# Optimization experiments

Measured on AMD Instinct MI355X. Metric: run time of the kernel, lower is better.

Reference implementation:

```python
import jax, jax.numpy as jnp
import numpy as np

N_NODES = 100000
N_EDGES = 800000
DIMS = [(768, 64), (64, 32), (32, 16), (16, 5)]


def setup_inputs() -> dict:
    key = jax.random.key(0)
    ks = jax.random.split(key, 3 + 3 * len(DIMS))
    inp = {
        "x": jax.random.normal(ks[0], (N_NODES, DIMS[0][0]), jnp.float32),
        "edge_index": jax.random.randint(ks[1], (2, N_EDGES), 0, N_NODES),
        "edge_weight": jax.random.uniform(ks[2], (N_EDGES,), jnp.float32),
    }
    for i, (di, do) in enumerate(DIMS, start=1):
        s = 1.0 / np.sqrt(di)
        k0, k1, k2 = ks[3 * i], ks[3 * i + 1], ks[3 * i + 2]
        inp[f"W{i}l"] = jax.random.uniform(k0, (di, do), jnp.float32, -s, s)
        inp[f"W{i}r"] = jax.random.uniform(k1, (di, do), jnp.float32, -s, s)
        inp[f"b{i}"] = jax.random.uniform(k2, (do,), jnp.float32, -s, s)
    return inp


def _sage_conv(h, src, dst, inv_deg, Wl, Wr, b):
    # SAGEConv (mean aggregation): lin_l(mean_{j->i} h_j) + lin_r(h_i)
    agg = jax.ops.segment_sum(h[src], dst, num_segments=h.shape[0]) * inv_deg[:, None]
    return agg @ Wl + h @ Wr + b


def reference(x, edge_index, edge_weight,
              W1l, W1r, b1, W2l, W2r, b2, W3l, W3r, b3, W4l, W4r, b4):
    # edge_weight is accepted (matches original forward) but PyG SAGEConv mean
    # aggregation ignores it. Dropout is identity (deterministic eval reference).
    src, dst = edge_index[0], edge_index[1]
    deg = jax.ops.segment_sum(jnp.ones((src.shape[0],), x.dtype), dst,
                              num_segments=x.shape[0])
    inv_deg = jnp.where(deg > 0, 1.0 / deg, 0.0)
    h = jax.nn.relu(_sage_conv(x, src, dst, inv_deg, W1l, W1r, b1))
    h = jax.nn.relu(_sage_conv(h, src, dst, inv_deg, W2l, W2r, b2))
    h = jax.nn.relu(_sage_conv(h, src, dst, inv_deg, W3l, W3r, b3))
    return _sage_conv(h, src, dst, inv_deg, W4l, W4r, b4)
```

## Files before the change

kernel.cpp:

```cpp
#include <hip/hip_runtime.h>

using half8 = __attribute__((ext_vector_type(8))) _Float16;
using f32x4 = __attribute__((ext_vector_type(4))) float;

typedef __attribute__((address_space(3))) unsigned int lds_uint;
typedef __attribute__((address_space(1))) const unsigned int glb_uint;
__device__ __forceinline__ void async_copy16(const void* g, void* l) {
  __builtin_amdgcn_global_load_lds((glb_uint*)g, (lds_uint*)l, 16, 0, 0);
}

__device__ __forceinline__ void raw_barrier() {
  asm volatile("" ::: "memory");
  __builtin_amdgcn_s_barrier();
  asm volatile("" ::: "memory");
}

__global__ void zero_kernel(int4* __restrict__ p, int n4) {
  int i = blockIdx.x * 256 + threadIdx.x;
  if (i < n4) p[i] = make_int4(0, 0, 0, 0);
}

__global__ void prep_all_kernel(const float* __restrict__ W1l, const float* __restrict__ W1r,
                                const float* __restrict__ W2l, const float* __restrict__ W2r,
                                const float* __restrict__ W3l, const float* __restrict__ W3r,
                                const float* __restrict__ W4l, const float* __restrict__ W4r,
                                _Float16* __restrict__ w1, _Float16* __restrict__ w2,
                                _Float16* __restrict__ w3, _Float16* __restrict__ w4) {
  int i = blockIdx.x * 256 + threadIdx.x;
  if (i < 98304) {
    int c = i / 768, k = i - c * 768;
    float v = (c < 64) ? W1l[k * 64 + c] : W1r[k * 64 + (c - 64)];
    w1[i] = (_Float16)v;
  } else if (i < 98304 + 4096) {
    int j = i - 98304;
    int c = j >> 6, k = j & 63;
    float v = (c < 32) ? W2l[k * 32 + c] : W2r[k * 32 + (c - 32)];
    w2[j] = (_Float16)v;
  } else if (i < 98304 + 4096 + 1024) {
    int j = i - (98304 + 4096);
    int c = j >> 5, k = j & 31;
    float v = (c < 16) ? W3l[k * 16 + c] : W3r[k * 16 + (c - 16)];
    w3[j] = (_Float16)v;
  } else if (i < 98304 + 4096 + 1024 + 512) {
    int j = i - (98304 + 4096 + 1024);
    int c = j >> 5, k = j & 31;
    float v = 0.f;
    if (k < 16) {
      if (c < 5) v = W4l[k * 5 + c];
      else if (c < 10) v = W4r[k * 5 + (c - 5)];
    }
    w4[j] = (_Float16)v;
  }
}

__global__ void deg_kernel(const int* __restrict__ dst, int* __restrict__ cnt, int e) {
  int i = blockIdx.x * 256 + threadIdx.x;
  if (i < e) atomicAdd(&cnt[dst[i]], 1);
}

__global__ void scan1_kernel(const int* __restrict__ cnt, int* __restrict__ off,
                             int* __restrict__ bsum, float* __restrict__ invd, int nodes) {
  __shared__ int sh[256];
  int tid = threadIdx.x;
  int base = blockIdx.x * 1024 + tid * 4;
  int a0 = (base + 0 < nodes) ? cnt[base + 0] : 0;
  int a1 = (base + 1 < nodes) ? cnt[base + 1] : 0;
  int a2 = (base + 2 < nodes) ? cnt[base + 2] : 0;
  int a3 = (base + 3 < nodes) ? cnt[base + 3] : 0;
  if (base + 0 < nodes) invd[base + 0] = a0 > 0 ? 1.0f / (float)a0 : 0.f;
  if (base + 1 < nodes) invd[base + 1] = a1 > 0 ? 1.0f / (float)a1 : 0.f;
  if (base + 2 < nodes) invd[base + 2] = a2 > 0 ? 1.0f / (float)a2 : 0.f;
  if (base + 3 < nodes) invd[base + 3] = a3 > 0 ? 1.0f / (float)a3 : 0.f;
  int s3 = a0 + a1 + a2 + a3;
  sh[tid] = s3;
  __syncthreads();
  for (int d = 1; d < 256; d <<= 1) {
    int v = (tid >= d) ? sh[tid - d] : 0;
    __syncthreads();
    sh[tid] += v;
    __syncthreads();
  }
  int excl = sh[tid] - s3;
  if (base + 0 <= nodes) off[base + 0] = excl;
  if (base + 1 <= nodes) off[base + 1] = excl + a0;
  if (base + 2 <= nodes) off[base + 2] = excl + a0 + a1;
  if (base + 3 <= nodes) off[base + 3] = excl + a0 + a1 + a2;
  if (tid == 255) bsum[blockIdx.x] = sh[255];
}

__global__ void scan2_kernel(int* __restrict__ bsum, int nb) {
  __shared__ int sh[128];
  int tid = threadIdx.x;
  int v = (tid < nb) ? bsum[tid] : 0;
  sh[tid] = v;
  __syncthreads();
  for (int d = 1; d < 128; d <<= 1) {
    int u = (tid >= d) ? sh[tid - d] : 0;
    __syncthreads();
    sh[tid] += u;
    __syncthreads();
  }
  if (tid < nb) bsum[tid] = sh[tid] - v;
}

__global__ void scan3_kernel(int* __restrict__ off, const int* __restrict__ bsum, int ntot) {
  int i = blockIdx.x * 256 + threadIdx.x;
  if (i < ntot) off[i] += bsum[i >> 10];
}

__global__ void sortfill_kernel(const int* __restrict__ src, const int* __restrict__ dst,
                                const int* __restrict__ off, int* __restrict__ cur,
                                int* __restrict__ csr, int e) {
  int i = blockIdx.x * 256 + threadIdx.x;
  if (i < e) {
    int d = dst[i];
    int pos = atomicAdd(&cur[d], 1);
    csr[off[d] + pos] = src[i];
  }
}

__global__ __launch_bounds__(256, 3) void gemm1_kernel(
    const float* __restrict__ x,
    const _Float16* __restrict__ w16,
    const float* __restrict__ bias,
    _Float16* __restrict__ p, _Float16* __restrict__ q, int n) {
  constexpr int DI = 768, BK = 32, NT = DI / BK;
  __shared__ float aS[3][64 * BK];
  __shared__ _Float16 bS[3][128 * BK];
  int t = threadIdx.x;
  int lane = t & 63, w = t >> 6;
  int lm = lane & 15, lk = lane >> 4;
  int m0 = blockIdx.x * 64;

  const float* agp[2];
  int abase[2];
#pragma unroll
  for (int j = 0; j < 2; ++j) {
    int g = j * 256 + w * 64 + lane;
    int row = g >> 3, gi = g & 7;
    int gj = gi ^ (row & 7);
    int grow = m0 + row;
    if (grow >= n) grow = n - 1;
    agp[j] = x + (size_t)grow * DI + gj * 4;
    abase[j] = (j * 256 + w * 64) * 4;
  }
  const _Float16* bgp[2];
  int bbase[2];
#pragma unroll
  for (int j = 0; j < 2; ++j) {
    int g = j * 256 + w * 64 + lane;
    int c = g >> 2, gi = g & 3;
    int gj = gi ^ ((c >> 1) & 3);
    bgp[j] = w16 + (size_t)c * DI + gj * 8;
    bbase[j] = (j * 256 + w * 64) * 8;
  }

  f32x4 acc[8];
#pragma unroll
  for (int ni = 0; ni < 8; ++ni) acc[ni] = (f32x4){0.f, 0.f, 0.f, 0.f};

  int r0l = w * 16 + lm;
  int sw = r0l & 7;
  int bsw = (lk ^ ((lm >> 1) & 3)) << 3;

  auto stage = [&](int buf, int kc) {
#pragma unroll
    for (int j = 0; j < 2; ++j) async_copy16(agp[j] + kc, &aS[buf][abase[j]]);
#pragma unroll
    for (int j = 0; j < 2; ++j) async_copy16(bgp[j] + kc, &bS[buf][bbase[j]]);
  };

  auto compute_tile = [&](const float* ab, const _Float16* bb) {
    f32x4 v0a = *(const f32x4*)(ab + r0l * 32 + (((lk * 2 + 0) ^ sw) << 2));
    f32x4 v0b = *(const f32x4*)(ab + r0l * 32 + (((lk * 2 + 1) ^ sw) << 2));
    half8 a0;
#pragma unroll
    for (int j = 0; j < 4; ++j) {
      a0[j] = (_Float16)v0a[j];
      a0[4 + j] = (_Float16)v0b[j];
    }
#pragma unroll
    for (int ni = 0; ni < 8; ++ni) {
      half8 b = *(const half8*)(bb + (ni * 16 + lm) * 32 + bsw);
      acc[ni] = __builtin_amdgcn_mfma_f32_16x16x32_f16(a0, b, acc[ni], 0, 0, 0);
    }
  };

  stage(0, 0);
  stage(1, BK);

  for (int ts = 0; ts < NT; ++ts) {
    if (ts + 2 < NT) {
      stage((ts + 2) % 3, (ts + 2) * BK);
      asm volatile("s_waitcnt vmcnt(8)" ::: "memory");
    } else if (ts + 1 < NT) {
      asm volatile("s_waitcnt vmcnt(4)" ::: "memory");
    } else {
      asm volatile("s_waitcnt vmcnt(0)" ::: "memory");
    }
    raw_barrier();
    int cur = ts % 3;
    compute_tile(aS[cur], bS[cur]);
    raw_barrier();
  }

#pragma unroll
  for (int ni = 0; ni < 8; ++ni) {
    int col = ni * 16 + lm;
#pragma unroll
    for (int j = 0; j < 4; ++j) {
      int row = m0 + w * 16 + lk * 4 + j;
      if (row < n) {
        float v = acc[ni][j];
        if (col < 64) p[(size_t)row * 64 + col] = (_Float16)v;
        else q[(size_t)row * 64 + (col - 64)] = (_Float16)(v + bias[col - 64]);
      }
    }
  }
}

template <int DIR, int DIP, int PSI, int NC, int NCR, int DO, int PSO>
__global__ __launch_bounds__(256) void fused_agg_gemm_kernel(
    const _Float16* __restrict__ pin, const _Float16* __restrict__ qin,
    const int* __restrict__ off, const int* __restrict__ csr, const float* __restrict__ invd,
    const _Float16* __restrict__ w16, const float* __restrict__ bias,
    _Float16* __restrict__ pout, _Float16* __restrict__ qout, int n) {
  constexpr int SP = DIP + 8;
  constexpr int C8 = DIR / 8;
  constexpr int CT = C8 / 2;
  constexpr int NF = NC / 16;
  __shared__ _Float16 hs[128 * SP];
  int t = threadIdx.x;
  int node_l = t >> 1, half = t & 1;
  int node = blockIdx.x * 128 + node_l;

  if (node < n) {
    int e0 = off[node], e1 = off[node + 1];
    const half8* p8 = (const half8*)pin;
    float s[CT][8];
#pragma unroll
    for (int c = 0; c < CT; ++c)
#pragma unroll
      for (int j = 0; j < 8; ++j) s[c][j] = 0.f;
    int e = e0;
    for (; e + 2 <= e1; e += 2) {
      int i0 = csr[e], i1 = csr[e + 1];
      half8 v0[CT], v1[CT];
#pragma unroll
      for (int c = 0; c < CT; ++c) v0[c] = p8[(size_t)i0 * PSI + half * CT + c];
#pragma unroll
      for (int c = 0; c < CT; ++c) v1[c] = p8[(size_t)i1 * PSI + half * CT + c];
#pragma unroll
      for (int c = 0; c < CT; ++c)
#pragma unroll
        for (int j = 0; j < 8; ++j) {
          s[c][j] += (float)v0[c][j];
          s[c][j] += (float)v1[c][j];
        }
    }
    if (e < e1) {
      int i0 = csr[e];
#pragma unroll
      for (int c = 0; c < CT; ++c) {
        half8 v = p8[(size_t)i0 * PSI + half * CT + c];
#pragma unroll
        for (int j = 0; j < 8; ++j) s[c][j] += (float)v[j];
      }
    }
    float id = invd[node];
#pragma unroll
    for (int c = 0; c < CT; ++c) {
      half8 qv = ((const half8*)qin)[(size_t)node * PSI + half * CT + c];
      half8 o;
#pragma unroll
      for (int j = 0; j < 8; ++j) o[j] = (_Float16)fmaxf(s[c][j] * id + (float)qv[j], 0.f);
      *(half8*)(hs + node_l * SP + (half * CT + c) * 8) = o;
    }
    if (DIP > DIR) {
      half8 z = {};
      *(half8*)(hs + node_l * SP + (C8 + half) * 8) = z;
    }
  }
  __syncthreads();

  int lane = t & 63, w = t >> 6;
  int lm = lane & 15, lk = lane >> 4;
  int r0l = w * 32 + lm, r1l = r0l + 16;
  const _Float16* wp = w16 + (size_t)lm * DIP + lk * 8;
  f32x4 acc[2][NF];
#pragma unroll
  for (int mi = 0; mi < 2; ++mi)
#pragma unroll
    for (int ni = 0; ni < NF; ++ni) acc[mi][ni] = (f32x4){0.f, 0.f, 0.f, 0.f};
#pragma unroll
  for (int kc = 0; kc < DIP; kc += 32) {
    half8 a0 = *(const half8*)(hs + r0l * SP + kc + lk * 8);
    half8 a1 = *(const half8*)(hs + r1l * SP + kc + lk * 8);
#pragma unroll
    for (int ni = 0; ni < NF; ++ni) {
      half8 b = *(const half8*)(wp + (size_t)ni * 16 * DIP + kc);
      acc[0][ni] = __builtin_amdgcn_mfma_f32_16x16x32_f16(a0, b, acc[0][ni], 0, 0, 0);
      acc[1][ni] = __builtin_amdgcn_mfma_f32_16x16x32_f16(a1, b, acc[1][ni], 0, 0, 0);
    }
  }
#pragma unroll
  for (int mi = 0; mi < 2; ++mi)
#pragma unroll
    for (int ni = 0; ni < NF; ++ni) {
      int col = ni * 16 + lm;
      if (col >= NCR) continue;
#pragma unroll
      for (int j = 0; j < 4; ++j) {
        int row = blockIdx.x * 128 + w * 32 + mi * 16 + lk * 4 + j;
        if (row < n) {
          float v = acc[mi][ni][j];
          if (col < DO) pout[(size_t)row * PSO + col] = (_Float16)v;
          else qout[(size_t)row * PSO + (col - DO)] = (_Float16)(v + bias[col - DO]);
        }
      }
    }
}

__global__ __launch_bounds__(256) void aggregate_last_kernel(
    const _Float16* __restrict__ p, const _Float16* __restrict__ q,
    const int* __restrict__ off, const int* __restrict__ csr,
    const float* __restrict__ invd, float* __restrict__ out, int n) {
  int node = blockIdx.x * 256 + threadIdx.x;
  if (node >= n) return;
  int e0 = off[node], e1 = off[node + 1];
  const half8* p8 = (const half8*)p;
  float s[8];
#pragma unroll
  for (int j = 0; j < 8; ++j) s[j] = 0.f;
  int e = e0;
  for (; e + 2 <= e1; e += 2) {
    half8 v0 = p8[csr[e]];
    half8 v1 = p8[csr[e + 1]];
#pragma unroll
    for (int j = 0; j < 8; ++j) {
      s[j] += (float)v0[j];
      s[j] += (float)v1[j];
    }
  }
  if (e < e1) {
    half8 v = p8[csr[e]];
#pragma unroll
    for (int j = 0; j < 8; ++j) s[j] += (float)v[j];
  }
  float id = invd[node];
  half8 qv = ((const half8*)q)[node];
#pragma unroll
  for (int j = 0; j < 5; ++j) out[(size_t)node * 5 + j] = s[j] * id + (float)qv[j];
}

extern "C" void kernel_launch(void* const* d_in, const int* in_sizes, int n_in,
                              void* d_out, int out_size, void* d_ws, size_t ws_size,
                              hipStream_t stream) {
  const float* x = (const float*)d_in[0];
  const int* ei = (const int*)d_in[1];
  const int E = in_sizes[1] / 2;
  const int* esrc = ei;
  const int* edst = ei + E;
  const float* W1l = (const float*)d_in[3];
  const float* W1r = (const float*)d_in[4];
  const float* b1 = (const float*)d_in[5];
  const float* W2l = (const float*)d_in[6];
  const float* W2r = (const float*)d_in[7];
  const float* b2 = (const float*)d_in[8];
  const float* W3l = (const float*)d_in[9];
  const float* W3r = (const float*)d_in[10];
  const float* b3 = (const float*)d_in[11];
  const float* W4l = (const float*)d_in[12];
  const float* W4r = (const float*)d_in[13];
  const float* b4 = (const float*)d_in[14];
  const int N = in_sizes[0] / 768;
  float* out = (float*)d_out;
  (void)n_in; (void)out_size; (void)ws_size;

  char* base = (char*)d_ws;
  size_t o = 0;
  auto alloc = [&](size_t bytes) -> void* {
    void* ptr = base + o;
    o = (o + bytes + 255) & ~(size_t)255;
    return ptr;
  };
  int* cnt = (int*)alloc((size_t)2 * N * 4);
  int* cur = cnt + N;
  int* off = (int*)alloc((size_t)(N + 1) * 4);
  int* bsum = (int*)alloc(1024);
  int* csr = (int*)alloc((size_t)E * 4);
  float* invd = (float*)alloc((size_t)N * 4);
  _Float16* w1 = (_Float16*)alloc((size_t)128 * 768 * 2);
  _Float16* w2 = (_Float16*)alloc((size_t)64 * 64 * 2);
  _Float16* w3 = (_Float16*)alloc((size_t)32 * 32 * 2);
  _Float16* w4 = (_Float16*)alloc((size_t)16 * 32 * 2);
  _Float16* P1 = (_Float16*)alloc((size_t)N * 64 * 2);
  _Float16* Q1 = (_Float16*)alloc((size_t)N * 64 * 2);
  _Float16* P2 = (_Float16*)alloc((size_t)N * 32 * 2);
  _Float16* Q2 = (_Float16*)alloc((size_t)N * 32 * 2);
  _Float16* P3 = (_Float16*)alloc((size_t)N * 16 * 2);
  _Float16* Q3 = (_Float16*)alloc((size_t)N * 16 * 2);
  _Float16* P4 = (_Float16*)alloc((size_t)N * 8 * 2);
  _Float16* Q4 = (_Float16*)alloc((size_t)N * 8 * 2);

  const int n4 = (2 * N + 3) / 4;
  zero_kernel<<<(n4 + 255) / 256, 256, 0, stream>>>((int4*)cnt, n4);
  prep_all_kernel<<<(98304 + 4096 + 1024 + 512 + 255) / 256, 256, 0, stream>>>(
      W1l, W1r, W2l, W2r, W3l, W3r, W4l, W4r, w1, w2, w3, w4);

  deg_kernel<<<(E + 255) / 256, 256, 0, stream>>>(edst, cnt, E);
  const int nb = (N + 1 + 1023) / 1024;
  scan1_kernel<<<nb, 256, 0, stream>>>(cnt, off, bsum, invd, N);
  scan2_kernel<<<1, 128, 0, stream>>>(bsum, nb);
  scan3_kernel<<<(N + 1 + 255) / 256, 256, 0, stream>>>(off, bsum, N + 1);
  sortfill_kernel<<<(E + 255) / 256, 256, 0, stream>>>(esrc, edst, off, cur, csr, E);

  gemm1_kernel<<<(N + 63) / 64, 256, 0, stream>>>(x, w1, b1, P1, Q1, N);
  const int gb = (N + 127) / 128;
  fused_agg_gemm_kernel<64, 64, 8, 64, 64, 32, 32>
      <<<gb, 256, 0, stream>>>(P1, Q1, off, csr, invd, w2, b2, P2, Q2, N);
  fused_agg_gemm_kernel<32, 32, 4, 32, 32, 16, 16>
      <<<gb, 256, 0, stream>>>(P2, Q2, off, csr, invd, w3, b3, P3, Q3, N);
  fused_agg_gemm_kernel<16, 32, 2, 16, 10, 5, 8>
      <<<gb, 256, 0, stream>>>(P3, Q3, off, csr, invd, w4, b4, P4, Q4, N);
  aggregate_last_kernel<<<(N + 255) / 256, 256, 0, stream>>>(P4, Q4, off, csr, invd, out, N);
}
```

Baseline: 273.5 us.

## Replace LDS-staged pipelined GEMM1 with direct global-to-register loads

Rewrites the first-layer GEMM to drop the triple-buffered async global-to-LDS staging and barriers, loading x rows and fp16 weights directly into registers per wave. Occupancy hint raised from 3 to 4 blocks per CU. This removes LDS traffic and barrier synchronisation but loses explicit prefetching and weight sharing across waves, relying on caches and occupancy to hide latency.

```diff
diff --git a/kernel.cpp b/kernel.cpp
--- a/kernel.cpp
+++ b/kernel.cpp
@@ -2,18 +2,6 @@
 
 using half8 = __attribute__((ext_vector_type(8))) _Float16;
 using f32x4 = __attribute__((ext_vector_type(4))) float;
-
-typedef __attribute__((address_space(3))) unsigned int lds_uint;
-typedef __attribute__((address_space(1))) const unsigned int glb_uint;
-__device__ __forceinline__ void async_copy16(const void* g, void* l) {
-  __builtin_amdgcn_global_load_lds((glb_uint*)g, (lds_uint*)l, 16, 0, 0);
-}
-
-__device__ __forceinline__ void raw_barrier() {
-  asm volatile("" ::: "memory");
-  __builtin_amdgcn_s_barrier();
-  asm volatile("" ::: "memory");
-}
 
 __global__ void zero_kernel(int4* __restrict__ p, int n4) {
   int i = blockIdx.x * 256 + threadIdx.x;
@@ -119,89 +107,40 @@
   }
 }
 
-__global__ __launch_bounds__(256, 3) void gemm1_kernel(
+__global__ __launch_bounds__(256, 4) void gemm1_kernel(
     const float* __restrict__ x,
     const _Float16* __restrict__ w16,
     const float* __restrict__ bias,
     _Float16* __restrict__ p, _Float16* __restrict__ q, int n) {
-  constexpr int DI = 768, BK = 32, NT = DI / BK;
-  __shared__ float aS[3][64 * BK];
-  __shared__ _Float16 bS[3][128 * BK];
-  int t = threadIdx.x;
-  int lane = t & 63, w = t >> 6;
+  constexpr int DI = 768;
+  int wave = threadIdx.x >> 6, lane = threadIdx.x & 63;
   int lm = lane & 15, lk = lane >> 4;
-  int m0 = blockIdx.x * 64;
-
-  const float* agp[2];
-  int abase[2];
-#pragma unroll
-  for (int j = 0; j < 2; ++j) {
-    int g = j * 256 + w * 64 + lane;
-    int row = g >> 3, gi = g & 7;
-    int gj = gi ^ (row & 7);
-    int grow = m0 + row;
-    if (grow >= n) grow = n - 1;
-    agp[j] = x + (size_t)grow * DI + gj * 4;
-    abase[j] = (j * 256 + w * 64) * 4;
-  }
-  const _Float16* bgp[2];
-  int bbase[2];
-#pragma unroll
-  for (int j = 0; j < 2; ++j) {
-    int g = j * 256 + w * 64 + lane;
-    int c = g >> 2, gi = g & 3;
-    int gj = gi ^ ((c >> 1) & 3);
-    bgp[j] = w16 + (size_t)c * DI + gj * 8;
-    bbase[j] = (j * 256 + w * 64) * 8;
-  }
+  int rbase = blockIdx.x * 64 + wave * 16;
+  int row = rbase + lm;
+  if (row >= n) row = n - 1;
+  const float* xr = x + (size_t)row * DI + lk * 8;
+  const _Float16* wp = w16 + (size_t)lm * DI + lk * 8;
 
   f32x4 acc[8];
 #pragma unroll
   for (int ni = 0; ni < 8; ++ni) acc[ni] = (f32x4){0.f, 0.f, 0.f, 0.f};
 
-  int r0l = w * 16 + lm;
-  int sw = r0l & 7;
-  int bsw = (lk ^ ((lm >> 1) & 3)) << 3;
-
-  auto stage = [&](int buf, int kc) {
-#pragma unroll
-    for (int j = 0; j < 2; ++j) async_copy16(agp[j] + kc, &aS[buf][abase[j]]);
-#pragma unroll
-    for (int j = 0; j < 2; ++j) async_copy16(bgp[j] + kc, &bS[buf][bbase[j]]);
-  };
-
-  auto compute_tile = [&](const float* ab, const _Float16* bb) {
-    f32x4 v0a = *(const f32x4*)(ab + r0l * 32 + (((lk * 2 + 0) ^ sw) << 2));
-    f32x4 v0b = *(const f32x4*)(ab + r0l * 32 + (((lk * 2 + 1) ^ sw) << 2));
-    half8 a0;
+#pragma unroll 1
+  for (int kc = 0; kc < DI; kc += 32) {
+    f32x4 xa = *(const f32x4*)(xr + kc);
+    f32x4 xb = *(const f32x4*)(xr + kc + 4);
+    half8 bf[8];
+#pragma unroll
+    for (int ni = 0; ni < 8; ++ni) bf[ni] = *(const half8*)(wp + (size_t)ni * 16 * DI + kc);
+    half8 a;
 #pragma unroll
     for (int j = 0; j < 4; ++j) {
-      a0[j] = (_Float16)v0a[j];
-      a0[4 + j] = (_Float16)v0b[j];
-    }
-#pragma unroll
-    for (int ni = 0; ni < 8; ++ni) {
-      half8 b = *(const half8*)(bb + (ni * 16 + lm) * 32 + bsw);
-      acc[ni] = __builtin_amdgcn_mfma_f32_16x16x32_f16(a0, b, acc[ni], 0, 0, 0);
-    }
-  };
-
-  stage(0, 0);
-  stage(1, BK);
-
-  for (int ts = 0; ts < NT; ++ts) {
-    if (ts + 2 < NT) {
-      stage((ts + 2) % 3, (ts + 2) * BK);
-      asm volatile("s_waitcnt vmcnt(8)" ::: "memory");
-    } else if (ts + 1 < NT) {
-      asm volatile("s_waitcnt vmcnt(4)" ::: "memory");
-    } else {
-      asm volatile("s_waitcnt vmcnt(0)" ::: "memory");
-    }
-    raw_barrier();
-    int cur = ts % 3;
-    compute_tile(aS[cur], bS[cur]);
-    raw_barrier();
+      a[j] = (_Float16)xa[j];
+      a[4 + j] = (_Float16)xb[j];
+    }
+#pragma unroll
+    for (int ni = 0; ni < 8; ++ni)
+      acc[ni] = __builtin_amdgcn_mfma_f32_16x16x32_f16(a, bf[ni], acc[ni], 0, 0, 0);
   }
 
 #pragma unroll
@@ -209,11 +148,11 @@
     int col = ni * 16 + lm;
 #pragma unroll
     for (int j = 0; j < 4; ++j) {
-      int row = m0 + w * 16 + lk * 4 + j;
-      if (row < n) {
+      int r = rbase + lk * 4 + j;
+      if (r < n) {
         float v = acc[ni][j];
-        if (col < 64) p[(size_t)row * 64 + col] = (_Float16)v;
-        else q[(size_t)row * 64 + (col - 64)] = (_Float16)(v + bias[col - 64]);
+        if (col < 64) p[(size_t)r * 64 + col] = (_Float16)v;
+        else q[(size_t)r * 64 + (col - 64)] = (_Float16)(v + bias[col - 64]);
       }
     }
   }
```

Result: slower. 376.9 us (+37.8%).
